# Optimization experiments

Measured on AMD Instinct MI355X. Metric: run time of the kernel, lower is better.

The kernel has to match this reference:

```python
import jax, jax.numpy as jnp
import numpy as np

B, N, HD = 128, 8192, 256


def setup_inputs() -> dict:
    key = jax.random.key(0)
    ks = jax.random.split(key, 12)
    s = 1.0 / np.sqrt(HD)
    return {
        "encoder_outputs": jax.random.normal(ks[0], (B, N, HD), jnp.float32),
        "hidden": jax.random.normal(ks[1], (B, HD), jnp.float32),
        "cell": jax.random.normal(ks[2], (B, HD), jnp.float32),
        "end_node_embed": jax.random.normal(ks[3], (1, HD), jnp.float32),
        "initial_input": jax.random.normal(ks[4], (B, 3 * HD), jnp.float32),
        # LSTMCell params (PyTorch layout: gates ordered i, f, g, o)
        "W_ih": jax.random.uniform(ks[5], (4 * HD, 3 * HD), jnp.float32, -s, s),
        "b_ih": jax.random.uniform(ks[6], (4 * HD,), jnp.float32, -s, s),
        "W_hh": jax.random.uniform(ks[7], (4 * HD, HD), jnp.float32, -s, s),
        "b_hh": jax.random.uniform(ks[8], (4 * HD,), jnp.float32, -s, s),
        # query_transform Linear params
        "Wq": jax.random.uniform(ks[9], (HD, HD), jnp.float32, -s, s),
        "bq": jax.random.uniform(ks[10], (HD,), jnp.float32, -s, s),
        "max_steps": 10,
    }


def reference(encoder_outputs, hidden, cell, end_node_embed, initial_input,
              W_ih, b_ih, W_hh, b_hh, Wq, bq, max_steps):
    # Prediction mode (teacher_indices=None): feed back top-3 gathered embeddings.
    def step(carry, _):
        h, c, x = carry
        gates = x @ W_ih.T + b_ih + h @ W_hh.T + b_hh        # (B, 4*HD)
        i, f, g, o = jnp.split(gates, 4, axis=-1)
        c_new = jax.nn.sigmoid(f) * c + jax.nn.sigmoid(i) * jnp.tanh(g)
        h_new = jax.nn.sigmoid(o) * jnp.tanh(c_new)
        query = h_new @ Wq.T + bq                            # (B, HD)
        logits = jnp.einsum('bd,bnd->bn', query, encoder_outputs)  # (B, N)
        _, top3 = jax.lax.top_k(logits, 3)                   # (B, 3) int32
        vecs = jnp.take_along_axis(encoder_outputs, top3[..., None], axis=1)  # (B, 3, HD)
        x_next = vecs.reshape(x.shape[0], -1)                # (B, 3*HD)
        return (h_new, c_new, x_next), (logits, top3)
    _, (logits_all, idx_all) = jax.lax.scan(
        step, (hidden, cell, initial_input), None, length=max_steps)
    return logits_all, idx_all  # (max_steps, B, N), (max_steps, B, 3)
```

## Files before the change

### kernel.cpp

```cpp
#include <hip/hip_runtime.h>

typedef unsigned short u16;
typedef unsigned int   u32;

#define B_    128
#define N_    8192
#define HD_   256
#define X_    768
#define T_    10
#define SEGS_ 32
#define SEGROWS_ 256

__device__ float g_h[B_*HD_];
__device__ float g_c[B_*HD_];
__device__ float g_q[B_*HD_];
__device__ float g_pval[B_*SEGS_*3];
__device__ int   g_pidx[B_*SEGS_*3];
__device__ int   g_isf32;

struct P {
  const void *enc, *h0, *c0, *x0, *Wih, *bih, *Whh, *bhh, *Wq, *bq;
  void* out;
};

#define LDSP(x) ((__attribute__((address_space(3))) void*)(x))
#define GLBP(x) ((const __attribute__((address_space(1))) void*)(x))

__device__ __forceinline__ float bf2f(u16 u){ return __uint_as_float(((u32)u)<<16); }
__device__ __forceinline__ float lo2f(u32 w){ return __uint_as_float(w<<16); }
__device__ __forceinline__ float hi2f(u32 w){ return __uint_as_float(w & 0xffff0000u); }
__device__ __forceinline__ u16 f2bf(float f){
  u32 u = __float_as_uint(f);
  u32 r = u + 0x7fffu + ((u>>16)&1u);
  return (u16)(r>>16);
}

template<bool F32>
__device__ __forceinline__ float ld1(const void* p, size_t i){
  if constexpr (F32) return ((const float*)p)[i];
  else               return bf2f(((const u16*)p)[i]);
}

template<bool F32>
__device__ __forceinline__ void st1(void* p, size_t i, float v){
  if constexpr (F32) ((float*)p)[i] = v;
  else               ((u16*)p)[i]   = f2bf(v);
}

template<bool F32>
__device__ __forceinline__ void ld8(const void* p, size_t i, float* o){
  if constexpr (F32){
    const float4* q = (const float4*)((const float*)p + i);
    float4 a = q[0], b = q[1];
    o[0]=a.x; o[1]=a.y; o[2]=a.z; o[3]=a.w;
    o[4]=b.x; o[5]=b.y; o[6]=b.z; o[7]=b.w;
  } else {
    uint4 u = *(const uint4*)((const u16*)p + i);
    o[0]=lo2f(u.x); o[1]=hi2f(u.x); o[2]=lo2f(u.y); o[3]=hi2f(u.y);
    o[4]=lo2f(u.z); o[5]=hi2f(u.z); o[6]=lo2f(u.w); o[7]=hi2f(u.w);
  }
}

__device__ __forceinline__ void t3ins(float v,int i,
    float&v0,int&i0,float&v1,int&i1,float&v2,int&i2){
  if (v>v0 || (v==v0 && i<i0)) { v2=v1;i2=i1; v1=v0;i1=i0; v0=v;i0=i; }
  else if (v>v1 || (v==v1 && i<i1)) { v2=v1;i2=i1; v1=v;i1=i; }
  else if (v>v2 || (v==v2 && i<i2)) { v2=v;i2=i; }
}

__global__ void k_probe(const void* enc){
  const int lane = threadIdx.x;
  const u16 u = ((const u16*)enc)[lane*2];
  const float a = fabsf(bf2f(u));
  const bool inr = (a >= 0.0009765625f) && (a <= 1024.0f);
  unsigned long long m = __ballot(inr ? 1 : 0);
  if (lane==0) g_isf32 = (__popcll(m) < 32) ? 1 : 0;
}

template<bool F32>
__device__ void lstm_b(const P& p, int t, int b)
{
  const int d = threadIdx.x;
  __shared__ float xs[X_];
  __shared__ float hs[HD_];
  __shared__ float hn[HD_];
  __shared__ int   idx3[3];

  float cd;
  if (t == 0){
    for (int i=d;i<X_;i+=256) xs[i] = ld1<F32>(p.x0, (size_t)b*X_+i);
    hs[d] = ld1<F32>(p.h0, (size_t)b*HD_+d);
    cd    = ld1<F32>(p.c0, (size_t)b*HD_+d);
  } else {
    if (d==0){
      float v0=-3.4e38f,v1=-3.4e38f,v2=-3.4e38f; int i0=-1,i1=-1,i2=-1;
      const float* pv = g_pval + b*SEGS_*3;
      const int*   pi = g_pidx + b*SEGS_*3;
      for (int s=0;s<SEGS_*3;s++) t3ins(pv[s],pi[s],v0,i0,v1,i1,v2,i2);
      idx3[0]=i0; idx3[1]=i1; idx3[2]=i2;
      const size_t ib = (size_t)T_*B_*N_ + (size_t)(t-1)*B_*3 + (size_t)b*3;
      st1<F32>(p.out, ib+0, (float)i0);
      st1<F32>(p.out, ib+1, (float)i1);
      st1<F32>(p.out, ib+2, (float)i2);
    }
    __syncthreads();
    #pragma unroll
    for (int j=0;j<3;j++){
      int jj = idx3[j]; jj = jj<0 ? 0 : (jj>N_-1 ? N_-1 : jj);
      xs[j*HD_+d] = ld1<F32>(p.enc, ((size_t)b*N_ + jj)*HD_ + d);
    }
    hs[d] = g_h[b*HD_+d];
    cd    = g_c[b*HD_+d];
  }
  __syncthreads();

  float g4[4];
  #pragma unroll
  for (int gi=0;gi<4;gi++){
    const int row = gi*HD_ + d;
    float acc = ld1<F32>(p.bih,row) + ld1<F32>(p.bhh,row);
    #pragma unroll 4
    for (int kk=0;kk<X_/8;kk++){
      float w[8]; ld8<F32>(p.Wih, (size_t)row*X_ + kk*8, w);
      #pragma unroll
      for (int j=0;j<8;j++) acc = fmaf(xs[kk*8+j], w[j], acc);
    }
    #pragma unroll 4
    for (int kk=0;kk<HD_/8;kk++){
      float w[8]; ld8<F32>(p.Whh, (size_t)row*HD_ + kk*8, w);
      #pragma unroll
      for (int j=0;j<8;j++) acc = fmaf(hs[kk*8+j], w[j], acc);
    }
    g4[gi]=acc;
  }
  const float sig_i = 1.f/(1.f+expf(-g4[0]));
  const float sig_f = 1.f/(1.f+expf(-g4[1]));
  const float tan_g = tanhf(g4[2]);
  const float sig_o = 1.f/(1.f+expf(-g4[3]));
  const float cn = sig_f*cd + sig_i*tan_g;
  const float hv = sig_o*tanhf(cn);
  g_c[b*HD_+d]=cn; g_h[b*HD_+d]=hv; hn[d]=hv;
  __syncthreads();

  float acc = ld1<F32>(p.bq,d);
  #pragma unroll 4
  for (int kk=0;kk<HD_/8;kk++){
    float w[8]; ld8<F32>(p.Wq, (size_t)d*HD_ + kk*8, w);
    #pragma unroll
    for (int j=0;j<8;j++) acc = fmaf(hn[kk*8+j], w[j], acc);
  }
  g_q[b*HD_+d]=acc;
}

__global__ __launch_bounds__(256) void k_lstm(P p, int t)
{
  if (g_isf32) lstm_b<true >(p, t, blockIdx.x);
  else         lstm_b<false>(p, t, blockIdx.x);
}

template<bool F32>
__device__ void logits_b(const P& p, int t, int b, int seg)
{
  __shared__ float qs[HD_];
  const int l = threadIdx.x;

  for (int i=l;i<HD_;i+=64) qs[i] = g_q[b*HD_+i];
  __syncthreads();

  float v0=-3.4e38f,v1=-3.4e38f,v2=-3.4e38f; int i0=-1,i1=-1,i2=-1;
  const int rowglob0 = seg*SEGROWS_;

  if constexpr (!F32){
    __shared__ uint4 buf[2][1024];
    const u16* encb = (const u16*)p.enc + ((size_t)b*N_ + (size_t)seg*SEGROWS_)*HD_;
    u16* outb = (u16*)p.out + (size_t)t*B_*N_ + (size_t)b*N_ + (size_t)seg*SEGROWS_;

    const int r  = l & 31;
    const int up = l >> 5;
    float res[8];

    #define STAGE(T) do{                                                      \
      const u16* s0 = encb + (size_t)(T)*32*HD_ + l*8;                        \
      _Pragma("unroll")                                                       \
      for (int i_=0;i_<16;i_++)                                               \
        __builtin_amdgcn_global_load_lds(GLBP(s0 + i_*512),                   \
                                         LDSP(&buf[(T)&1][i_*64]), 16, 0, 0); \
    }while(0)

    #define COMP(T) do{                                                       \
      const uint4* rowp = &buf[(T)&1][r*32];                                  \
      float acc_ = 0.f;                                                       \
      _Pragma("unroll")                                                       \
      for (int j_=0;j_<16;j_++){                                              \
        const int s_ = ((j_ + r) & 15) + up*16;                               \
        uint4 u_ = rowp[s_];                                                  \
        const float* qk_ = &qs[s_*8];                                         \
        acc_ = fmaf(lo2f(u_.x), qk_[0], acc_);                                \
        acc_ = fmaf(hi2f(u_.x), qk_[1], acc_);                                \
        acc_ = fmaf(lo2f(u_.y), qk_[2], acc_);                                \
        acc_ = fmaf(hi2f(u_.y), qk_[3], acc_);                                \
        acc_ = fmaf(lo2f(u_.z), qk_[4], acc_);                                \
        acc_ = fmaf(hi2f(u_.z), qk_[5], acc_);                                \
        acc_ = fmaf(lo2f(u_.w), qk_[6], acc_);                                \
        acc_ = fmaf(hi2f(u_.w), qk_[7], acc_);                                \
      }                                                                       \
      acc_ += __shfl_xor(acc_, 32, 64);                                       \
      res[T] = acc_;                                                          \
    }while(0)

    STAGE(0);
    #pragma unroll
    for (int T=0;T<7;T++){
      STAGE(T+1);
      asm volatile("s_waitcnt vmcnt(16)" ::: "memory");
      COMP(T);
    }
    asm volatile("s_waitcnt vmcnt(0)" ::: "memory");
    COMP(7);
    #undef STAGE
    #undef COMP

    if (l < 32){
      #pragma unroll
      for (int T=0;T<8;T++){
        t3ins(res[T], rowglob0 + T*32 + r, v0,i0,v1,i1,v2,i2);
        outb[T*32 + r] = f2bf(res[T]);
      }
    }
  } else {
    const float* encb = (const float*)p.enc + ((size_t)b*N_ + (size_t)seg*SEGROWS_)*HD_;
    float* outb = (float*)p.out + (size_t)t*B_*N_ + (size_t)b*N_ + (size_t)seg*SEGROWS_;
    for (int row=l; row<SEGROWS_; row+=64){
      const float4* rp = (const float4*)(encb + (size_t)row*HD_);
      float acc = 0.f;
      #pragma unroll 8
      for (int k=0;k<64;k++){
        float4 v = rp[k];
        const float* qk = &qs[k*4];
        acc = fmaf(v.x, qk[0], acc);
        acc = fmaf(v.y, qk[1], acc);
        acc = fmaf(v.z, qk[2], acc);
        acc = fmaf(v.w, qk[3], acc);
      }
      t3ins(acc, rowglob0 + row, v0,i0,v1,i1,v2,i2);
      outb[row] = acc;
    }
  }

  #pragma unroll
  for (int d=1; d<64; d<<=1){
    float w0=__shfl_xor(v0,d,64), w1=__shfl_xor(v1,d,64), w2=__shfl_xor(v2,d,64);
    int   j0=__shfl_xor(i0,d,64), j1=__shfl_xor(i1,d,64), j2=__shfl_xor(i2,d,64);
    t3ins(w0,j0, v0,i0,v1,i1,v2,i2);
    t3ins(w1,j1, v0,i0,v1,i1,v2,i2);
    t3ins(w2,j2, v0,i0,v1,i1,v2,i2);
  }
  if (l==0){
    float* pv = g_pval + (b*SEGS_+seg)*3;
    int*   pi = g_pidx + (b*SEGS_+seg)*3;
    pv[0]=v0; pv[1]=v1; pv[2]=v2;
    pi[0]=i0; pi[1]=i1; pi[2]=i2;
  }
}

__global__ __launch_bounds__(64) void k_logits(P p, int t)
{
  const int b   = blockIdx.x >> 5;
  const int seg = blockIdx.x & 31;
  if (g_isf32) logits_b<true >(p, t, b, seg);
  else         logits_b<false>(p, t, b, seg);
}

template<bool F32>
__device__ void final_b(const P& p, int b)
{
  if (threadIdx.x==0){
    float v0=-3.4e38f,v1=-3.4e38f,v2=-3.4e38f; int i0=-1,i1=-1,i2=-1;
    const float* pv = g_pval + b*SEGS_*3;
    const int*   pi = g_pidx + b*SEGS_*3;
    for (int s=0;s<SEGS_*3;s++) t3ins(pv[s],pi[s],v0,i0,v1,i1,v2,i2);
    const size_t ib = (size_t)T_*B_*N_ + (size_t)(T_-1)*B_*3 + (size_t)b*3;
    st1<F32>(p.out, ib+0, (float)i0);
    st1<F32>(p.out, ib+1, (float)i1);
    st1<F32>(p.out, ib+2, (float)i2);
  }
}

__global__ void k_final(P p)
{
  if (g_isf32) final_b<true >(p, blockIdx.x);
  else         final_b<false>(p, blockIdx.x);
}

extern "C" void kernel_launch(void* const* d_in, const int* in_sizes, int n_in,
                              void* d_out, int out_size, void* d_ws, size_t ws_size,
                              hipStream_t stream)
{
  (void)in_sizes; (void)n_in; (void)out_size; (void)d_ws; (void)ws_size;
  P p;
  p.enc = d_in[0];
  p.h0  = d_in[1];
  p.c0  = d_in[2];
  p.x0  = d_in[4];
  p.Wih = d_in[5];
  p.bih = d_in[6];
  p.Whh = d_in[7];
  p.bhh = d_in[8];
  p.Wq  = d_in[9];
  p.bq  = d_in[10];
  p.out = d_out;

  k_probe<<<dim3(1),dim3(64),0,stream>>>(p.enc);

  for (int t=0;t<T_;t++){
    k_lstm  <<<dim3(B_),        dim3(256),0,stream>>>(p, t);
    k_logits<<<dim3(B_*SEGS_),  dim3(64), 0,stream>>>(p, t);
  }
  k_final<<<dim3(B_),dim3(64),0,stream>>>(p);
}
```

Measured before the change: 4.424 ms.

## Fuse all timesteps into one cooperative persistent kernel with grid syncs

Replaces the per-step LSTM and logits kernel launches with a single cooperative kernel. It loops over timesteps and phases (LSTM gates, query projection, logits/top-3), separated by grid-wide syncs. LSTM work is split into 64-thread blocks over quarters of the hidden dimension, h is double-buffered, and logits segments grow from 256 to 1024 rows with top-3 folded into the streaming loop. This is meant to remove launch overhead and tail effects. The cost is fewer segments (less parallelism per batch), redundant top-3 merges in every quarter-block, and grid-sync latency. A multi-launch fallback path is kept.

```diff
diff --git a/kernel.cpp b/kernel.cpp
--- a/kernel.cpp
+++ b/kernel.cpp
@@ -1,4 +1,7 @@
 #include <hip/hip_runtime.h>
+#include <hip/hip_cooperative_groups.h>
+
+namespace cg = cooperative_groups;
 
 typedef unsigned short u16;
 typedef unsigned int   u32;
@@ -8,10 +11,10 @@
 #define HD_   256
 #define X_    768
 #define T_    10
-#define SEGS_ 32
-#define SEGROWS_ 256
-
-__device__ float g_h[B_*HD_];
+#define SEGS_ 8
+#define SEGROWS_ 1024
+
+__device__ float g_hh[2][B_*HD_];
 __device__ float g_c[B_*HD_];
 __device__ float g_q[B_*HD_];
 __device__ float g_pval[B_*SEGS_*3];
@@ -22,6 +25,10 @@
   const void *enc, *h0, *c0, *x0, *Wih, *bih, *Whh, *bhh, *Wq, *bq;
   void* out;
 };
+
+struct SmemLG { uint4 buf[2][1024]; float qs[HD_]; };
+struct SmemLS { float xs[X_]; float hs[HD_]; };
+union Smem { SmemLG lg; SmemLS ls; };
 
 #define LDSP(x) ((__attribute__((address_space(3))) void*)(x))
 #define GLBP(x) ((const __attribute__((address_space(1))) void*)(x))
@@ -78,39 +85,38 @@
 }
 
 template<bool F32>
-__device__ void lstm_b(const P& p, int t, int b)
-{
-  const int d = threadIdx.x;
-  __shared__ float xs[X_];
-  __shared__ float hs[HD_];
-  __shared__ float hn[HD_];
-  __shared__ int   idx3[3];
-
+__device__ void phaseA(const P& p, int t, int vb, Smem& sm)
+{
+  const int b = vb>>2, qt = vb&3, l = threadIdx.x;
+  const int d = qt*64 + l;
+  float* xs = sm.ls.xs;
+  float* hs = sm.ls.hs;
   float cd;
-  if (t == 0){
-    for (int i=d;i<X_;i+=256) xs[i] = ld1<F32>(p.x0, (size_t)b*X_+i);
-    hs[d] = ld1<F32>(p.h0, (size_t)b*HD_+d);
-    cd    = ld1<F32>(p.c0, (size_t)b*HD_+d);
+  if (t==0){
+    for (int i=l;i<X_;i+=64)  xs[i] = ld1<F32>(p.x0,(size_t)b*X_+i);
+    for (int i=l;i<HD_;i+=64) hs[i] = ld1<F32>(p.h0,(size_t)b*HD_+i);
+    cd = ld1<F32>(p.c0,(size_t)b*HD_+d);
   } else {
-    if (d==0){
-      float v0=-3.4e38f,v1=-3.4e38f,v2=-3.4e38f; int i0=-1,i1=-1,i2=-1;
-      const float* pv = g_pval + b*SEGS_*3;
-      const int*   pi = g_pidx + b*SEGS_*3;
-      for (int s=0;s<SEGS_*3;s++) t3ins(pv[s],pi[s],v0,i0,v1,i1,v2,i2);
-      idx3[0]=i0; idx3[1]=i1; idx3[2]=i2;
-      const size_t ib = (size_t)T_*B_*N_ + (size_t)(t-1)*B_*3 + (size_t)b*3;
-      st1<F32>(p.out, ib+0, (float)i0);
-      st1<F32>(p.out, ib+1, (float)i1);
-      st1<F32>(p.out, ib+2, (float)i2);
-    }
-    __syncthreads();
+    float v0=-3.4e38f,v1=-3.4e38f,v2=-3.4e38f; int i0=-1,i1=-1,i2=-1;
+    const float* pv = g_pval + b*SEGS_*3;
+    const int*   pi = g_pidx + b*SEGS_*3;
+    for (int s=0;s<SEGS_*3;s++) t3ins(pv[s],pi[s],v0,i0,v1,i1,v2,i2);
+    if (qt==0 && l==0){
+      const size_t ib=(size_t)T_*B_*N_+(size_t)(t-1)*B_*3+(size_t)b*3;
+      st1<F32>(p.out,ib+0,(float)i0);
+      st1<F32>(p.out,ib+1,(float)i1);
+      st1<F32>(p.out,ib+2,(float)i2);
+    }
+    int j3[3];
+    j3[0] = i0<0?0:(i0>N_-1?N_-1:i0);
+    j3[1] = i1<0?0:(i1>N_-1?N_-1:i1);
+    j3[2] = i2<0?0:(i2>N_-1?N_-1:i2);
     #pragma unroll
-    for (int j=0;j<3;j++){
-      int jj = idx3[j]; jj = jj<0 ? 0 : (jj>N_-1 ? N_-1 : jj);
-      xs[j*HD_+d] = ld1<F32>(p.enc, ((size_t)b*N_ + jj)*HD_ + d);
-    }
-    hs[d] = g_h[b*HD_+d];
-    cd    = g_c[b*HD_+d];
+    for (int j=0;j<3;j++)
+      for (int i=l;i<HD_;i+=64)
+        xs[j*HD_+i] = ld1<F32>(p.enc, ((size_t)b*N_+j3[j])*HD_+i);
+    for (int i=l;i<HD_;i+=64) hs[i] = g_hh[t&1][b*HD_+i];
+    cd = g_c[b*HD_+d];
   }
   __syncthreads();
 
@@ -121,63 +127,64 @@
     float acc = ld1<F32>(p.bih,row) + ld1<F32>(p.bhh,row);
     #pragma unroll 4
     for (int kk=0;kk<X_/8;kk++){
-      float w[8]; ld8<F32>(p.Wih, (size_t)row*X_ + kk*8, w);
+      float w[8]; ld8<F32>(p.Wih,(size_t)row*X_+kk*8,w);
       #pragma unroll
-      for (int j=0;j<8;j++) acc = fmaf(xs[kk*8+j], w[j], acc);
+      for (int j=0;j<8;j++) acc=fmaf(xs[kk*8+j],w[j],acc);
     }
     #pragma unroll 4
     for (int kk=0;kk<HD_/8;kk++){
-      float w[8]; ld8<F32>(p.Whh, (size_t)row*HD_ + kk*8, w);
+      float w[8]; ld8<F32>(p.Whh,(size_t)row*HD_+kk*8,w);
       #pragma unroll
-      for (int j=0;j<8;j++) acc = fmaf(hs[kk*8+j], w[j], acc);
+      for (int j=0;j<8;j++) acc=fmaf(hs[kk*8+j],w[j],acc);
     }
     g4[gi]=acc;
   }
-  const float sig_i = 1.f/(1.f+expf(-g4[0]));
-  const float sig_f = 1.f/(1.f+expf(-g4[1]));
-  const float tan_g = tanhf(g4[2]);
-  const float sig_o = 1.f/(1.f+expf(-g4[3]));
-  const float cn = sig_f*cd + sig_i*tan_g;
-  const float hv = sig_o*tanhf(cn);
-  g_c[b*HD_+d]=cn; g_h[b*HD_+d]=hv; hn[d]=hv;
-  __syncthreads();
-
+  const float si_=1.f/(1.f+expf(-g4[0]));
+  const float sf_=1.f/(1.f+expf(-g4[1]));
+  const float tg_=tanhf(g4[2]);
+  const float so_=1.f/(1.f+expf(-g4[3]));
+  const float cn = sf_*cd + si_*tg_;
+  const float hv = so_*tanhf(cn);
+  g_c[b*HD_+d]          = cn;
+  g_hh[(t+1)&1][b*HD_+d]= hv;
+  __syncthreads();
+}
+
+template<bool F32>
+__device__ void phaseQ(const P& p, int t, int vb, Smem& sm)
+{
+  const int b=vb>>2, qt=vb&3, l=threadIdx.x, d=qt*64+l;
+  float* hs = sm.ls.hs;
+  for (int i=l;i<HD_;i+=64) hs[i]=g_hh[(t+1)&1][b*HD_+i];
+  __syncthreads();
   float acc = ld1<F32>(p.bq,d);
   #pragma unroll 4
   for (int kk=0;kk<HD_/8;kk++){
-    float w[8]; ld8<F32>(p.Wq, (size_t)d*HD_ + kk*8, w);
+    float w[8]; ld8<F32>(p.Wq,(size_t)d*HD_+kk*8,w);
     #pragma unroll
-    for (int j=0;j<8;j++) acc = fmaf(hn[kk*8+j], w[j], acc);
+    for (int j=0;j<8;j++) acc=fmaf(hs[kk*8+j],w[j],acc);
   }
   g_q[b*HD_+d]=acc;
-}
-
-__global__ __launch_bounds__(256) void k_lstm(P p, int t)
-{
-  if (g_isf32) lstm_b<true >(p, t, blockIdx.x);
-  else         lstm_b<false>(p, t, blockIdx.x);
-}
-
-template<bool F32>
-__device__ void logits_b(const P& p, int t, int b, int seg)
-{
-  __shared__ float qs[HD_];
-  const int l = threadIdx.x;
-
-  for (int i=l;i<HD_;i+=64) qs[i] = g_q[b*HD_+i];
+  __syncthreads();
+}
+
+template<bool F32>
+__device__ void phaseB(const P& p, int t, int vb, Smem& sm)
+{
+  const int b=vb>>3, seg=vb&7, l=threadIdx.x;
+  float* qs = sm.lg.qs;
+  for (int i=l;i<HD_;i+=64) qs[i]=g_q[b*HD_+i];
   __syncthreads();
 
   float v0=-3.4e38f,v1=-3.4e38f,v2=-3.4e38f; int i0=-1,i1=-1,i2=-1;
   const int rowglob0 = seg*SEGROWS_;
 
   if constexpr (!F32){
-    __shared__ uint4 buf[2][1024];
-    const u16* encb = (const u16*)p.enc + ((size_t)b*N_ + (size_t)seg*SEGROWS_)*HD_;
+    uint4 (*buf)[1024] = sm.lg.buf;
+    const u16* encb = (const u16*)p.enc + ((size_t)b*N_+(size_t)seg*SEGROWS_)*HD_;
     u16* outb = (u16*)p.out + (size_t)t*B_*N_ + (size_t)b*N_ + (size_t)seg*SEGROWS_;
-
     const int r  = l & 31;
     const int up = l >> 5;
-    float res[8];
 
     #define STAGE(T) do{                                                      \
       const u16* s0 = encb + (size_t)(T)*32*HD_ + l*8;                        \
@@ -186,7 +193,6 @@
         __builtin_amdgcn_global_load_lds(GLBP(s0 + i_*512),                   \
                                          LDSP(&buf[(T)&1][i_*64]), 16, 0, 0); \
     }while(0)
-
     #define COMP(T) do{                                                       \
       const uint4* rowp = &buf[(T)&1][r*32];                                  \
       float acc_ = 0.f;                                                       \
@@ -205,30 +211,25 @@
         acc_ = fmaf(hi2f(u_.w), qk_[7], acc_);                                \
       }                                                                       \
       acc_ += __shfl_xor(acc_, 32, 64);                                       \
-      res[T] = acc_;                                                          \
+      if (l < 32){                                                            \
+        t3ins(acc_, rowglob0 + (T)*32 + r, v0,i0,v1,i1,v2,i2);                \
+        outb[(T)*32 + r] = f2bf(acc_);                                        \
+      }                                                                       \
     }while(0)
 
     STAGE(0);
-    #pragma unroll
-    for (int T=0;T<7;T++){
+    #pragma unroll 1
+    for (int T=0;T<31;T++){
       STAGE(T+1);
       asm volatile("s_waitcnt vmcnt(16)" ::: "memory");
       COMP(T);
     }
     asm volatile("s_waitcnt vmcnt(0)" ::: "memory");
-    COMP(7);
+    COMP(31);
     #undef STAGE
     #undef COMP
-
-    if (l < 32){
-      #pragma unroll
-      for (int T=0;T<8;T++){
-        t3ins(res[T], rowglob0 + T*32 + r, v0,i0,v1,i1,v2,i2);
-        outb[T*32 + r] = f2bf(res[T]);
-      }
-    }
   } else {
-    const float* encb = (const float*)p.enc + ((size_t)b*N_ + (size_t)seg*SEGROWS_)*HD_;
+    const float* encb = (const float*)p.enc + ((size_t)b*N_+(size_t)seg*SEGROWS_)*HD_;
     float* outb = (float*)p.out + (size_t)t*B_*N_ + (size_t)b*N_ + (size_t)seg*SEGROWS_;
     for (int row=l; row<SEGROWS_; row+=64){
       const float4* rp = (const float4*)(encb + (size_t)row*HD_);
@@ -261,36 +262,57 @@
     pv[0]=v0; pv[1]=v1; pv[2]=v2;
     pi[0]=i0; pi[1]=i1; pi[2]=i2;
   }
-}
-
-__global__ __launch_bounds__(64) void k_logits(P p, int t)
-{
-  const int b   = blockIdx.x >> 5;
-  const int seg = blockIdx.x & 31;
-  if (g_isf32) logits_b<true >(p, t, b, seg);
-  else         logits_b<false>(p, t, b, seg);
-}
-
-template<bool F32>
-__device__ void final_b(const P& p, int b)
+  __syncthreads();
+}
+
+template<bool F32>
+__device__ void phaseF(const P& p, int vb)
 {
   if (threadIdx.x==0){
     float v0=-3.4e38f,v1=-3.4e38f,v2=-3.4e38f; int i0=-1,i1=-1,i2=-1;
-    const float* pv = g_pval + b*SEGS_*3;
-    const int*   pi = g_pidx + b*SEGS_*3;
+    const float* pv = g_pval + vb*SEGS_*3;
+    const int*   pi = g_pidx + vb*SEGS_*3;
     for (int s=0;s<SEGS_*3;s++) t3ins(pv[s],pi[s],v0,i0,v1,i1,v2,i2);
-    const size_t ib = (size_t)T_*B_*N_ + (size_t)(T_-1)*B_*3 + (size_t)b*3;
+    const size_t ib = (size_t)T_*B_*N_ + (size_t)(T_-1)*B_*3 + (size_t)vb*3;
     st1<F32>(p.out, ib+0, (float)i0);
     st1<F32>(p.out, ib+1, (float)i1);
     st1<F32>(p.out, ib+2, (float)i2);
   }
 }
 
-__global__ void k_final(P p)
-{
-  if (g_isf32) final_b<true >(p, blockIdx.x);
-  else         final_b<false>(p, blockIdx.x);
-}
+template<bool F32>
+__device__ void coop_run(const P& p, int nb)
+{
+  __shared__ Smem sm;
+  cg::grid_group grid = cg::this_grid();
+  for (int t=0;t<T_;t++){
+    for (int vb=blockIdx.x; vb<512; vb+=nb)       phaseA<F32>(p,t,vb,sm);
+    grid.sync();
+    for (int vb=blockIdx.x; vb<512; vb+=nb)       phaseQ<F32>(p,t,vb,sm);
+    grid.sync();
+    for (int vb=blockIdx.x; vb<B_*SEGS_; vb+=nb)  phaseB<F32>(p,t,vb,sm);
+    grid.sync();
+  }
+  for (int vb=blockIdx.x; vb<B_; vb+=nb)          phaseF<F32>(p,vb);
+}
+
+__global__ __launch_bounds__(64) void k_all(P p, int nb)
+{
+  if (g_isf32) coop_run<true >(p,nb);
+  else         coop_run<false>(p,nb);
+}
+
+__global__ __launch_bounds__(64) void k_pA(P p, int t)
+{ __shared__ Smem sm;
+  if (g_isf32) phaseA<true >(p,t,blockIdx.x,sm); else phaseA<false>(p,t,blockIdx.x,sm); }
+__global__ __launch_bounds__(64) void k_pQ(P p, int t)
+{ __shared__ Smem sm;
+  if (g_isf32) phaseQ<true >(p,t,blockIdx.x,sm); else phaseQ<false>(p,t,blockIdx.x,sm); }
+__global__ __launch_bounds__(64) void k_pB(P p, int t)
+{ __shared__ Smem sm;
+  if (g_isf32) phaseB<true >(p,t,blockIdx.x,sm); else phaseB<false>(p,t,blockIdx.x,sm); }
+__global__ __launch_bounds__(64) void k_pF(P p)
+{ if (g_isf32) phaseF<true >(p,blockIdx.x); else phaseF<false>(p,blockIdx.x); }
 
 extern "C" void kernel_launch(void* const* d_in, const int* in_sizes, int n_in,
                               void* d_out, int out_size, void* d_ws, size_t ws_size,
@@ -312,9 +334,26 @@
 
   k_probe<<<dim3(1),dim3(64),0,stream>>>(p.enc);
 
-  for (int t=0;t<T_;t++){
-    k_lstm  <<<dim3(B_),        dim3(256),0,stream>>>(p, t);
-    k_logits<<<dim3(B_*SEGS_),  dim3(64), 0,stream>>>(p, t);
-  }
-  k_final<<<dim3(B_),dim3(64),0,stream>>>(p);
-}
+  int occ = 0;
+  hipError_t oe = hipOccupancyMaxActiveBlocksPerMultiprocessor(&occ, k_all, 64, 0);
+  bool done = false;
+  if (oe == hipSuccess && occ > 0){
+    int nb = occ * 256;
+    if (nb > B_*SEGS_) nb = B_*SEGS_;
+    if (nb >= 64){
+      void* args[] = { (void*)&p, (void*)&nb };
+      hipError_t le = hipLaunchCooperativeKernel((void*)k_all, dim3(nb), dim3(64),
+                                                 args, 0, stream);
+      done = (le == hipSuccess);
+    }
+  }
+
+  if (!done){
+    for (int t=0;t<T_;t++){
+      k_pA<<<dim3(512),      dim3(64),0,stream>>>(p, t);
+      k_pQ<<<dim3(512),      dim3(64),0,stream>>>(p, t);
+      k_pB<<<dim3(B_*SEGS_), dim3(64),0,stream>>>(p, t);
+    }
+    k_pF<<<dim3(B_),dim3(64),0,stream>>>(p);
+  }
+}
```

After: 5.910 ms. 1.34x slower.
